# Performance work log

Measured on AMD Instinct MI355X. Metric: run time of the kernel, lower is better.

The kernel has to match this reference:

```python
import jax, jax.numpy as jnp
import numpy as np

N, E = 8000, 96000
S, V, G = 128, 64, 64          # scalar channels, l=1 vector channels, gate channels
LAT, OH = 128, 64
D = S + 3 * V                  # 320 feature dim per node/edge
AVG_NEIGH = 12.0
EPS = 1e-8

def _split(x):
    return x[:, :S], x[:, S:].reshape(x.shape[0], V, 3)

def sep_layernorm(x, ws, bs, wv):
    # separable LN: layernorm on l=0 scalars, component RMS norm on l=1 vectors
    s, v = _split(x)
    mu = jnp.mean(s, -1, keepdims=True)
    sc = s - mu
    s = sc * jax.lax.rsqrt(jnp.mean(sc * sc, -1, keepdims=True) + EPS) * ws + bs
    v = v * jax.lax.rsqrt(jnp.mean(v * v, (-2, -1), keepdims=True) + EPS) * wv[:, None]
    return s, v

def edge_frame(ev):
    # orthonormal frame with first axis along the edge (SO2 m=0 axis)
    a = ev * jax.lax.rsqrt(jnp.sum(ev * ev, -1, keepdims=True) + EPS)
    ref = jnp.where(jnp.abs(a[:, :1]) < 0.9,
                    jnp.array([1.0, 0.0, 0.0], ev.dtype),
                    jnp.array([0.0, 1.0, 0.0], ev.dtype))
    b = jnp.cross(a, ref)
    b = b * jax.lax.rsqrt(jnp.sum(b * b, -1, keepdims=True) + EPS)
    c = jnp.cross(a, b)
    return jnp.stack([a, b, c], axis=1)  # [E,3,3], rows are frame axes

def gate_act(s_all, v, n_s, n_g):
    s, g = s_all[:, :n_s], s_all[:, n_s:n_s + n_g]
    return jax.nn.silu(s), jax.nn.sigmoid(g)[:, :, None] * v

def e3_linear(s, v, ws, bs, wv):
    s = s @ ws * (1.0 / np.sqrt(s.shape[-1])) + bs
    v = jnp.einsum('eum,uk->ekm', v, wv) * (1.0 / np.sqrt(v.shape[1]))
    return s, v

def setup_inputs() -> dict:
    key = jax.random.key(0)
    ks = jax.random.split(key, 20)
    f = jnp.float32
    p = lambda k, sh: jax.random.normal(k, sh, f)
    inp = {}
    inp['latents'] = p(ks[0], (E, LAT))
    inp['node_features'] = p(ks[1], (N, D))
    inp['edge_features'] = p(ks[2], (E, D))
    at = jax.random.randint(ks[3], (N,), 0, OH)
    inp['atom_type'] = at
    inp['node_onehot'] = jax.nn.one_hot(at, OH, dtype=f)
    inp['edge_index'] = jax.random.randint(ks[4], (2, E), 0, N)
    inp['edge_vector'] = p(ks[5], (E, 3))
    inp['active_edges'] = jnp.arange(E)
    inp['sln_n_ws'] = jnp.ones((S,), f); inp['sln_n_bs'] = jnp.zeros((S,), f); inp['sln_n_wv'] = jnp.ones((V,), f)
    inp['sln_e_ws'] = jnp.ones((S,), f); inp['sln_e_bs'] = jnp.zeros((S,), f); inp['sln_e_wv'] = jnp.ones((V,), f)
    inp['so2_w0'] = p(ks[6], (3 * S + 3 * V, S + G + V))
    inp['so2_w1r'] = p(ks[7], (3 * V, V))
    inp['so2_w1i'] = p(ks[8], (3 * V, V))
    inp['env_w'] = p(ks[9], (LAT, S + V))
    inp['lp_ws'] = p(ks[10], (S, S)); inp['lp_bs'] = jnp.zeros((S,), f); inp['lp_wv'] = p(ks[11], (V, V))
    inp['oh_w_ss'] = p(ks[12], (S, OH, S))
    inp['oh_w_sg'] = p(ks[13], (S, OH, G))
    inp['oh_w_vv'] = p(ks[14], (V, OH, V))
    inp['ohl_ws'] = p(ks[15], (S, S)); inp['ohl_bs'] = jnp.zeros((S,), f); inp['ohl_wv'] = p(ks[16], (V, V))
    inp['res_param'] = jnp.zeros((1,), f)
    return inp

def reference(latents, node_features, edge_features, atom_type, node_onehot,
              edge_index, edge_vector, active_edges,
              sln_n_ws, sln_n_bs, sln_n_wv, sln_e_ws, sln_e_bs, sln_e_wv,
              so2_w0, so2_w1r, so2_w1i, env_w,
              lp_ws, lp_bs, lp_wv,
              oh_w_ss, oh_w_sg, oh_w_vv, ohl_ws, ohl_bs, ohl_wv, res_param):
    ctr = edge_index[0][active_edges]
    nbr = edge_index[1][active_edges]
    ns, nv = sep_layernorm(node_features, sln_n_ws, sln_n_bs, sln_n_wv)
    es, evf = sep_layernorm(edge_features, sln_e_ws, sln_e_bs, sln_e_wv)
    # concat center | edge | neighbor (scalars and vectors kept separate)
    sc = jnp.concatenate([ns[ctr], es, ns[nbr]], -1)          # [E, 3S]
    vc = jnp.concatenate([nv[ctr], evf, nv[nbr]], 1)          # [E, 3V, 3]
    R = edge_frame(edge_vector[active_edges])
    vf = jnp.einsum('eij,euj->eui', R, vc)                    # rotate into edge frame
    # SO2 linear: m=0 mixes scalars + on-axis components; m=+-1 mix with (re,im) weights
    m0_in = jnp.concatenate([sc, vf[:, :, 0]], -1)            # [E, 3S+3V]
    m0_out = m0_in @ so2_w0 * (1.0 / np.sqrt(m0_in.shape[-1]))  # [E, S+G+V]
    n1 = 1.0 / np.sqrt(vf.shape[1])
    vp = (vf[:, :, 1] @ so2_w1r - vf[:, :, 2] @ so2_w1i) * n1
    vm = (vf[:, :, 1] @ so2_w1i + vf[:, :, 2] @ so2_w1r) * n1
    v_out = jnp.stack([m0_out[:, S + G:], vp, vm], -1)        # [E,V,3] in frame
    v_out = jnp.einsum('eij,eui->euj', R, v_out)              # rotate back
    # gate activation + post linear
    ms, mv = gate_act(m0_out[:, :S + G], v_out, S, G)
    ms, mv = e3_linear(ms, mv, lp_ws, lp_bs, lp_wv)
    # env weighting (E3ElementLinear with weights from latents) + scatter to centers
    w = latents[active_edges] @ env_w * (1.0 / np.sqrt(LAT))  # [E, S+V]
    ms = ms * w[:, :S]
    mv = mv * w[:, S:, None]
    inv = 1.0 / np.sqrt(AVG_NEIGH)
    agg_s = jax.ops.segment_sum(ms, ctr, num_segments=N) * inv
    agg_v = jax.ops.segment_sum(mv, ctr, num_segments=N) * inv
    # one-hot FullyConnectedTensorProduct -> gate -> linear
    n_ss = 1.0 / np.sqrt(S * OH)
    n_vv = 1.0 / np.sqrt(V * OH)
    t_s = jnp.einsum('nu,nv,uvk->nk', agg_s, node_onehot, oh_w_ss) * n_ss
    t_g = jnp.einsum('nu,nv,uvk->nk', agg_s, node_onehot, oh_w_sg) * n_ss
    t_v = jnp.einsum('num,nv,uvk->nkm', agg_v, node_onehot, oh_w_vv) * n_vv
    gs, gv = gate_act(jnp.concatenate([t_s, t_g], -1), t_v, S, G)
    os_, ov = e3_linear(gs, gv, ohl_ws, ohl_bs, ohl_wv)
    new = jnp.concatenate([os_, ov.reshape(-1, 3 * V)], -1)
    # residual mixing (identity residual since node_irreps_in == irreps_out)
    alpha = jax.nn.sigmoid(res_param)[0]
    return alpha * node_features + (1.0 - alpha) * new
```

## Files before the change

### kernel.cpp

```cpp
#include <hip/hip_runtime.h>

#define EPS_LN 1e-8f

typedef __bf16 bf16x8 __attribute__((ext_vector_type(8)));
typedef float  f32x4  __attribute__((ext_vector_type(4)));

__device__ __forceinline__ float sigmoidf_(float x){ return 1.0f/(1.0f+__expf(-x)); }
__device__ __forceinline__ float siluf_(float x){ return x*sigmoidf_(x); }
__device__ __forceinline__ unsigned short f2bf(float x){ union{ __bf16 b; unsigned short u;} c; c.b = (__bf16)x; return c.u; }
__device__ __forceinline__ float bf2f(unsigned short u){ return __uint_as_float(((unsigned)u)<<16); }

union F4 { float4 v; float f[4]; };

__device__ __forceinline__ void st_bf4(char* base, int row, int stride_bytes, int k,
                                       float x0, float x1, float x2, float x3){
    union { __bf16 h[4]; unsigned long long u; } p;
    p.h[0]=(__bf16)x0; p.h[1]=(__bf16)x1; p.h[2]=(__bf16)x2; p.h[3]=(__bf16)x3;
    *(unsigned long long*)(base + row*stride_bytes + ((2*k) ^ ((row&7)<<4))) = p.u;
}
__device__ __forceinline__ bf16x8 ld_frag(const char* base, int row, int stride_bytes, int kbyte){
    return *(const bf16x8*)(base + row*stride_bytes + (kbyte ^ ((row&7)<<4)));
}
__device__ __forceinline__ void st_g4(__bf16* p, float x0, float x1, float x2, float x3){
    union { __bf16 h[4]; unsigned long long u; } pk;
    pk.h[0]=(__bf16)x0; pk.h[1]=(__bf16)x1; pk.h[2]=(__bf16)x2; pk.h[3]=(__bf16)x3;
    *(unsigned long long*)p = pk.u;
}
__device__ __forceinline__ uint4 pack8(float4 a, float4 b){
    union { __bf16 h[8]; uint4 u; } p;
    p.h[0]=(__bf16)a.x; p.h[1]=(__bf16)a.y; p.h[2]=(__bf16)a.z; p.h[3]=(__bf16)a.w;
    p.h[4]=(__bf16)b.x; p.h[5]=(__bf16)b.y; p.h[6]=(__bf16)b.z; p.h[7]=(__bf16)b.w;
    return p.u;
}
__device__ __forceinline__ int fm_idx(int n, int k, int NKT){
    return ((n>>4)*NKT + (k>>5))*512 + ((k>>3)&3)*128 + (n&15)*8 + (k&7);
}

__global__ void prep_weights(const float* __restrict__ w0,
                             const float* __restrict__ w1r, const float* __restrict__ w1i,
                             const float* __restrict__ env_w, const float* __restrict__ lp_ws,
                             const float* __restrict__ lp_wv,
                             __bf16* __restrict__ Wt, __bf16* __restrict__ w1rt, __bf16* __restrict__ w1it,
                             __bf16* __restrict__ Wfm, __bf16* __restrict__ Bvfm,
                             __bf16* __restrict__ envfm, __bf16* __restrict__ lpsfm,
                             __bf16* __restrict__ lpvfm)
{
    int t = blockIdx.x*256 + threadIdx.x;
    if (t < 576*256){
        int n = t/576, k = t%576;
        float v = w0[(size_t)k*256 + n];
        Wt[t] = (__bf16)v;
        Wfm[fm_idx(n,k,18)] = (__bf16)v;
    }
    if (t < 64*192){
        int c = t/192, k = t%192;
        w1rt[t] = (__bf16)w1r[(size_t)k*64 + c];
        w1it[t] = (__bf16)w1i[(size_t)k*64 + c];
    }
    if (t < 128*384){
        int n = t/384, k = t%384;
        float v;
        if (n < 64) v = (k<192) ? w1r[(size_t)k*64+n] : -w1i[(size_t)(k-192)*64+n];
        else        v = (k<192) ? w1i[(size_t)k*64+(n-64)] : w1r[(size_t)(k-192)*64+(n-64)];
        Bvfm[fm_idx(n,k,12)] = (__bf16)v;
    }
    if (t < 192*128){ int n=t/128, k=t%128; envfm[fm_idx(n,k,4)] = (__bf16)env_w[(size_t)k*192+n]; }
    if (t < 128*128){ int n=t/128, k=t%128; lpsfm[fm_idx(n,k,4)] = (__bf16)lp_ws[(size_t)k*128+n]; }
    if (t < 64*64)  { int n=t/64,  k=t%64;  lpvfm[fm_idx(n,k,2)] = (__bf16)lp_wv[(size_t)k*64+n]; }
}

__global__ void prep_oh(const float* __restrict__ oh_ss, const float* __restrict__ oh_sg,
                        const float* __restrict__ oh_vv,
                        __bf16* __restrict__ ssT, __bf16* __restrict__ sgT, __bf16* __restrict__ vvT)
{
    int t = blockIdx.x*256 + threadIdx.x;
    if (t < 64*128*128){
        int at = t / 16384;
        int r  = t & 16383;
        int u = r >> 7, k = r & 127;
        ssT[t] = (__bf16)oh_ss[((size_t)u*64 + at)*128 + k];
    }
    if (t < 64*128*64){
        int at = t / 8192;
        int r  = t & 8191;
        int u = r >> 6, k = r & 63;
        sgT[t] = (__bf16)oh_sg[((size_t)u*64 + at)*64 + k];
    }
    if (t < 64*64*64){
        int at = t / 4096;
        int r  = t & 4095;
        int u = r >> 6, k = r & 63;
        vvT[t] = (__bf16)oh_vv[((size_t)u*64 + at)*64 + k];
    }
}

__global__ void csr_count(const int* __restrict__ ei, const int* __restrict__ act,
                          int* __restrict__ cnt, int EA)
{
    int e = blockIdx.x*256 + threadIdx.x;
    if (e < EA) atomicAdd(&cnt[ei[act[e]]], 1);
}
__global__ void csr_scan(const int* __restrict__ cnt, int* __restrict__ offs,
                         int* __restrict__ cursor, int N)
{
    __shared__ int part[256];
    int t = threadIdx.x;
    int chunk = (N + 255) / 256;
    int lo = t*chunk, hi = lo+chunk; if (hi > N) hi = N; if (lo > N) lo = N;
    int s = 0;
    for (int i=lo;i<hi;i++) s += cnt[i];
    part[t] = s;
    __syncthreads();
    for (int d=1; d<256; d<<=1){
        int v = (t>=d) ? part[t-d] : 0;
        __syncthreads();
        part[t] += v;
        __syncthreads();
    }
    int run = (t==0) ? 0 : part[t-1];
    for (int i=lo;i<hi;i++){
        offs[i] = run; cursor[i] = run;
        run += cnt[i];
    }
    if (t==255) offs[N] = part[255];
}
__global__ void csr_fill(const int* __restrict__ ei, const int* __restrict__ act,
                         int* __restrict__ cursor, int* __restrict__ elist, int EA)
{
    int e = blockIdx.x*256 + threadIdx.x;
    if (e < EA){
        int n = ei[act[e]];
        int p = atomicAdd(&cursor[n], 1);
        elist[p] = e;
    }
}

__global__ void node_ln_kernel(const float* __restrict__ nf,
                               const float* __restrict__ ws, const float* __restrict__ bs,
                               const float* __restrict__ wv,
                               float* __restrict__ ns, float* __restrict__ nv, int N)
{
    int t = threadIdx.x;
    int lane = t & 63;
    int n = blockIdx.x*4 + (t>>6);
    if (n >= N) return;
    const float* row = nf + (size_t)n*320;
    float s0 = row[lane], s1 = row[64+lane];
    float sum = s0+s1, sq = s0*s0+s1*s1;
    #pragma unroll
    for (int m=1;m<64;m<<=1){ sum += __shfl_xor(sum,m,64); sq += __shfl_xor(sq,m,64); }
    float mu = sum*(1.0f/128.0f);
    float rs = rsqrtf(sq*(1.0f/128.0f) - mu*mu + EPS_LN);
    ns[(size_t)n*128+lane]    = (s0-mu)*rs*ws[lane]    + bs[lane];
    ns[(size_t)n*128+64+lane] = (s1-mu)*rs*ws[64+lane] + bs[64+lane];
    float v0 = row[128+lane], v1 = row[192+lane], v2 = row[256+lane];
    float vs = v0*v0+v1*v1+v2*v2;
    #pragma unroll
    for (int m=1;m<64;m<<=1) vs += __shfl_xor(vs,m,64);
    float rv = rsqrtf(vs*(1.0f/192.0f) + EPS_LN);
    nv[(size_t)n*192+lane]     = v0*rv*wv[lane/3];
    nv[(size_t)n*192+64+lane]  = v1*rv*wv[(64+lane)/3];
    nv[(size_t)n*192+128+lane] = v2*rv*wv[(128+lane)/3];
}

__global__ void stage_kernel(
    const float* __restrict__ ef_all,
    const int*   __restrict__ edge_index,
    const float* __restrict__ edge_vector,
    const int*   __restrict__ active_edges,
    const float* __restrict__ e_ws, const float* __restrict__ e_bs, const float* __restrict__ e_wv,
    const float* __restrict__ ns, const float* __restrict__ nv,
    __bf16* __restrict__ m0in, __bf16* __restrict__ vfg,
    float* __restrict__ Rg,
    int EA, int EF)
{
    int tid = blockIdx.x*256 + threadIdx.x;
    int e = tid >> 4, l = tid & 15;
    if (e >= EA) return;
    int ae = active_edges[e];
    int ct = edge_index[ae];
    int nb = edge_index[EF + ae];
    float ex = edge_vector[(size_t)ae*3+0];
    float ey = edge_vector[(size_t)ae*3+1];
    float ez = edge_vector[(size_t)ae*3+2];
    float rn = rsqrtf(ex*ex+ey*ey+ez*ez + EPS_LN);
    float ax = ex*rn, ay = ey*rn, az = ez*rn;
    float rx, ry;
    if (fabsf(ax) < 0.9f) { rx = 1.0f; ry = 0.0f; } else { rx = 0.0f; ry = 1.0f; }
    float bx = -az*ry, by = az*rx, bz = ax*ry - ay*rx;
    float bn = rsqrtf(bx*bx+by*by+bz*bz + EPS_LN);
    bx*=bn; by*=bn; bz*=bn;
    float cx = ay*bz - az*by;
    float cy = az*bx - ax*bz;
    float cz = ax*by - ay*bx;
    if (l == 0){
        float* Rr = Rg + (size_t)e*12;
        *(float4*)(Rr)   = make_float4(ax,ay,az,bx);
        *(float4*)(Rr+4) = make_float4(by,bz,cx,cy);
        *(float4*)(Rr+8) = make_float4(cz,0.f,0.f,0.f);
    }
    __bf16* Arow = m0in + (size_t)e*576;
    __bf16* V1r  = vfg + (size_t)e*384;
    __bf16* V2r  = V1r + 192;
    {
        const float4* pc4 = (const float4*)(ns + (size_t)ct*128);
        const float4* pn4 = (const float4*)(ns + (size_t)nb*128);
        F4 a,b2,c,d;
        a.v = pc4[l]; b2.v = pc4[16+l]; c.v = pn4[l]; d.v = pn4[16+l];
        st_g4(Arow + l*4,       a.f[0],a.f[1],a.f[2],a.f[3]);
        st_g4(Arow + 64 + l*4,  b2.f[0],b2.f[1],b2.f[2],b2.f[3]);
        st_g4(Arow + 256 + l*4, c.f[0],c.f[1],c.f[2],c.f[3]);
        st_g4(Arow + 320 + l*4, d.f[0],d.f[1],d.f[2],d.f[3]);
    }
    const float* ef = ef_all + (size_t)e*320;
    {
        F4 sa, sb;
        sa.v = *(const float4*)(ef + l*4);
        sb.v = *(const float4*)(ef + 64 + l*4);
        float sum=0.f, sq=0.f;
        #pragma unroll
        for (int i=0;i<4;i++){ sum += sa.f[i]+sb.f[i]; sq += sa.f[i]*sa.f[i]+sb.f[i]*sb.f[i]; }
        #pragma unroll
        for (int m=1;m<16;m<<=1){ sum += __shfl_xor(sum,m,64); sq += __shfl_xor(sq,m,64); }
        float mu = sum*(1.0f/128.0f);
        float rs = rsqrtf(sq*(1.0f/128.0f)-mu*mu + EPS_LN);
        float o0[4], o1[4];
        #pragma unroll
        for (int i=0;i<4;i++){
            int c0 = l*4+i, c1 = 64+l*4+i;
            o0[i] = (sa.f[i]-mu)*rs*e_ws[c0]+e_bs[c0];
            o1[i] = (sb.f[i]-mu)*rs*e_ws[c1]+e_bs[c1];
        }
        st_g4(Arow + 128 + l*4, o0[0],o0[1],o0[2],o0[3]);
        st_g4(Arow + 192 + l*4, o1[0],o1[1],o1[2],o1[3]);
    }
    {
        F4 va, vb, vc;
        va.v = *(const float4*)(ef + 128 + l*12);
        vb.v = *(const float4*)(ef + 128 + l*12 + 4);
        vc.v = *(const float4*)(ef + 128 + l*12 + 8);
        float vv[12];
        #pragma unroll
        for (int i=0;i<4;i++){ vv[i]=va.f[i]; vv[4+i]=vb.f[i]; vv[8+i]=vc.f[i]; }
        float sq=0.f;
        #pragma unroll
        for (int i=0;i<12;i++) sq += vv[i]*vv[i];
        #pragma unroll
        for (int m=1;m<16;m<<=1) sq += __shfl_xor(sq,m,64);
        float rv = rsqrtf(sq*(1.0f/192.0f) + EPS_LN);
        float f0[4], f1[4], f2[4];
        #pragma unroll
        for (int j=0;j<4;j++){
            int u = 4*l + j;
            float sc = rv * e_wv[u];
            float x = vv[3*j]*sc, y = vv[3*j+1]*sc, z = vv[3*j+2]*sc;
            f0[j] = ax*x+ay*y+az*z;
            f1[j] = bx*x+by*y+bz*z;
            f2[j] = cx*x+cy*y+cz*z;
        }
        st_g4(Arow + 384 + 64 + 4*l, f0[0],f0[1],f0[2],f0[3]);
        st_g4(V1r + 64 + 4*l, f1[0],f1[1],f1[2],f1[3]);
        st_g4(V2r + 64 + 4*l, f2[0],f2[1],f2[2],f2[3]);
    }
    {
        const float* pv = nv + (size_t)ct*192 + l*12;
        F4 va, vb, vc;
        va.v = *(const float4*)(pv);
        vb.v = *(const float4*)(pv+4);
        vc.v = *(const float4*)(pv+8);
        float vv[12];
        #pragma unroll
        for (int i=0;i<4;i++){ vv[i]=va.f[i]; vv[4+i]=vb.f[i]; vv[8+i]=vc.f[i]; }
        float f0[4], f1[4], f2[4];
        #pragma unroll
        for (int j=0;j<4;j++){
            float x = vv[3*j], y = vv[3*j+1], z = vv[3*j+2];
            f0[j] = ax*x+ay*y+az*z;
            f1[j] = bx*x+by*y+bz*z;
            f2[j] = cx*x+cy*y+cz*z;
        }
        st_g4(Arow + 384 + 4*l, f0[0],f0[1],f0[2],f0[3]);
        st_g4(V1r + 4*l, f1[0],f1[1],f1[2],f1[3]);
        st_g4(V2r + 4*l, f2[0],f2[1],f2[2],f2[3]);
    }
    {
        const float* pv = nv + (size_t)nb*192 + l*12;
        F4 va, vb, vc;
        va.v = *(const float4*)(pv);
        vb.v = *(const float4*)(pv+4);
        vc.v = *(const float4*)(pv+8);
        float vv[12];
        #pragma unroll
        for (int i=0;i<4;i++){ vv[i]=va.f[i]; vv[4+i]=vb.f[i]; vv[8+i]=vc.f[i]; }
        float f0[4], f1[4], f2[4];
        #pragma unroll
        for (int j=0;j<4;j++){
            float x = vv[3*j], y = vv[3*j+1], z = vv[3*j+2];
            f0[j] = ax*x+ay*y+az*z;
            f1[j] = bx*x+by*y+bz*z;
            f2[j] = cx*x+cy*y+cz*z;
        }
        st_g4(Arow + 384 + 128 + 4*l, f0[0],f0[1],f0[2],f0[3]);
        st_g4(V1r + 128 + 4*l, f1[0],f1[1],f1[2],f1[3]);
        st_g4(V2r + 128 + 4*l, f2[0],f2[1],f2[2],f2[3]);
    }
}

enum { EPI_PLAIN=0, EPI_LPS=1, EPI_LPV=2 };

template<int N, int K, int RT, int EPI, bool AGATHER>
__global__ __launch_bounds__((N/64)*RT*64)
void gemm_k(const __bf16* __restrict__ Ag, const float* __restrict__ Agf,
            const int* __restrict__ aidx,
            const __bf16* __restrict__ Bfm,
            unsigned short* __restrict__ outp,
            const unsigned short* __restrict__ wenv,
            const float* __restrict__ bias,
            float scale, int M)
{
    constexpr int NT  = N/64;
    constexpr int BM  = RT*64;
    constexpr int T   = NT*RT*64;
    constexpr int NKT = K/32;
    constexpr int NK  = K/64;
    constexpr int CA  = (BM*8 + T - 1)/T;
    __shared__ __align__(16) char lA[2][BM*128];

    const int tid  = threadIdx.x;
    const int brow = blockIdx.x*BM;
    const int mpl  = blockIdx.y;
    const __bf16* A = AGATHER ? nullptr : (Ag + (size_t)mpl*M*K);

    uint4 ra[CA];
    auto loadA = [&](int ks){
        #pragma unroll
        for (int i=0;i<CA;i++){
            int c = tid + i*T;
            if (c < BM*8){
                int r = c>>3;
                int gr = brow + r; if (gr >= M) gr = M-1;
                if constexpr (AGATHER){
                    int ae = aidx[gr];
                    const float* base = Agf + (size_t)ae*K + ks*64 + (c&7)*8;
                    float4 f0 = *(const float4*)(base);
                    float4 f1 = *(const float4*)(base+4);
                    ra[i] = pack8(f0, f1);
                } else {
                    ra[i] = *(const uint4*)((const char*)(A + (size_t)gr*K + ks*64) + (c&7)*16);
                }
            }
        }
    };
    auto storeA = [&](int buf){
        #pragma unroll
        for (int i=0;i<CA;i++){
            int c = tid + i*T;
            if (c < BM*8){
                int r = c>>3, off = (c&7)*16;
                *(uint4*)(&lA[buf][r*128 + (off ^ ((r&7)<<4))]) = ra[i];
            }
        }
    };

    const int wid = tid>>6, ln = tid&63;
    const int cc = ln & 15, gq = ln >> 4;
    const int wn = wid % NT, wm = wid / NT;
    const __bf16* bbase = Bfm + ((size_t)wn*4*NKT)*512 + (size_t)ln*8;

    f32x4 acc[4][4];
    #pragma unroll
    for (int i=0;i<4;i++)
        #pragma unroll
        for (int j=0;j<4;j++) acc[i][j] = (f32x4){0,0,0,0};

    loadA(0); storeA(0);
    int cur = 0;
    for (int ks=0; ks<NK; ks++){
        __syncthreads();
        if (ks+1 < NK) loadA(ks+1);
        #pragma unroll
        for (int kt2=0;kt2<2;kt2++){
            const int kt = ks*2 + kt2;
            const int kb = kt2*64 + 16*gq;
            bf16x8 af[4];
            #pragma unroll
            for (int mf=0;mf<4;mf++){
                int r = wm*64 + mf*16 + cc;
                af[mf] = *(const bf16x8*)(&lA[cur][r*128 + (kb ^ ((r&7)<<4))]);
            }
            #pragma unroll
            for (int nf=0;nf<4;nf++){
                bf16x8 bfr = *(const bf16x8*)(bbase + ((size_t)nf*NKT + kt)*512);
                #pragma unroll
                for (int mf=0;mf<4;mf++)
                    acc[mf][nf] = __builtin_amdgcn_mfma_f32_16x16x32_bf16(af[mf], bfr, acc[mf][nf], 0,0,0);
            }
        }
        if (ks+1 < NK) storeA(cur^1);
        cur ^= 1;
    }

    const float inv_avg_ = 0.288675134595f;
    #pragma unroll
    for (int mf=0;mf<4;mf++){
        #pragma unroll
        for (int nf=0;nf<4;nf++){
            #pragma unroll
            for (int j=0;j<4;j++){
                int gr = brow + wm*64 + mf*16 + gq*4 + j;
                if (gr >= M) continue;
                int col = wn*64 + nf*16 + cc;
                float v = acc[mf][nf][j];
                if constexpr (EPI == EPI_PLAIN){
                    outp[(size_t)gr*N + col] = f2bf(v*scale);
                } else if constexpr (EPI == EPI_LPS){
                    float val = (v*scale + bias[col]) * bf2f(wenv[(size_t)gr*192 + col]) * inv_avg_;
                    outp[(size_t)gr*320 + col] = f2bf(val);
                } else {
                    float val = v*0.125f * bf2f(wenv[(size_t)gr*192 + 128 + col]) * inv_avg_;
                    outp[(size_t)gr*320 + 128 + mpl*64 + col] = f2bf(val);
                }
            }
        }
    }
}

__global__ void mid_kernel(const unsigned short* __restrict__ m0out,
                           const unsigned short* __restrict__ vpvm,
                           const float* __restrict__ Rg,
                           unsigned short* __restrict__ As,
                           unsigned short* __restrict__ MVp, int EA)
{
    int tid = blockIdx.x*256 + threadIdx.x;
    int e = tid>>6, u = tid&63;
    if (e >= EA) return;
    float rl = (u < 12) ? Rg[(size_t)e*12 + u] : 0.f;
    float R0=__shfl(rl,0,64), R1=__shfl(rl,1,64), R2=__shfl(rl,2,64);
    float R3=__shfl(rl,3,64), R4=__shfl(rl,4,64), R5=__shfl(rl,5,64);
    float R6=__shfl(rl,6,64), R7=__shfl(rl,7,64), R8=__shfl(rl,8,64);
    const unsigned short* mo = m0out + (size_t)e*256;
    float s0 = bf2f(mo[192 + u]);
    float gt = sigmoidf_(bf2f(mo[128 + u]));
    float p  = bf2f(vpvm[(size_t)e*128 + u]);
    float q  = bf2f(vpvm[(size_t)e*128 + 64 + u]);
    size_t eu = (size_t)e*64 + u;
    size_t P  = (size_t)EA*64;
    MVp[eu]       = f2bf(gt*(R0*s0 + R3*p + R6*q));
    MVp[P + eu]   = f2bf(gt*(R1*s0 + R4*p + R7*q));
    MVp[2*P + eu] = f2bf(gt*(R2*s0 + R5*p + R8*q));
    As[(size_t)e*128 + u]      = f2bf(siluf_(bf2f(mo[u])));
    As[(size_t)e*128 + 64 + u] = f2bf(siluf_(bf2f(mo[64 + u])));
}

__launch_bounds__(256, 3)
__global__ void edge_kernel_fused(
    const float* __restrict__ latents,
    const float* __restrict__ ef_all,
    const int*   __restrict__ edge_index,
    const float* __restrict__ edge_vector,
    const int*   __restrict__ active_edges,
    const float* __restrict__ e_ws, const float* __restrict__ e_bs, const float* __restrict__ e_wv,
    const __bf16* __restrict__ Wt,
    const __bf16* __restrict__ w1rt,
    const __bf16* __restrict__ w1it,
    const float* __restrict__ env_w,
    const float* __restrict__ lp_ws, const float* __restrict__ lp_bs, const float* __restrict__ lp_wv,
    const float* __restrict__ ns, const float* __restrict__ nv,
    unsigned short* __restrict__ eout,
    int EA, int EF)
{
    __shared__ __align__(16) char smem[46592];
    char* sAbC = smem;
    char* sVFC = smem + 18432;
    float* sO  = (float*)smem;
    float* MV  = (float*)(smem + 16640);
    float* WE  = (float*)(smem + 33280);
    float* sR  = (float*)(smem + 45824);

    const int t = threadIdx.x;
    const int g = t >> 4, l = t & 15;
    const int e = blockIdx.x*16 + g;
    const bool act = (e < EA);

    int ct = 0, ae = 0;

    if (act) {
        ae = active_edges[e];
        ct = edge_index[ae];
        int nb = edge_index[EF + ae];
        float ex = edge_vector[(size_t)ae*3+0];
        float ey = edge_vector[(size_t)ae*3+1];
        float ez = edge_vector[(size_t)ae*3+2];
        float rn = rsqrtf(ex*ex+ey*ey+ez*ez + EPS_LN);
        float ax = ex*rn, ay = ey*rn, az = ez*rn;
        float rx, ry;
        if (fabsf(ax) < 0.9f) { rx = 1.0f; ry = 0.0f; } else { rx = 0.0f; ry = 1.0f; }
        float bx = -az*ry, by = az*rx, bz = ax*ry - ay*rx;
// ... 224 lines not shown
                        wacc[i]   += la.f[kk]*e0v.f[i];
                        wacc[4+i] += la.f[kk]*e1v.f[i];
                        wacc[8+i] += la.f[kk]*e2v.f[i];
                    }
                }
            }
            const float inv128 = 0.0883883476483f;
            #pragma unroll
            for (int i=0;i<12;i++) WE[g*196 + cc2 + i] = wacc[i]*inv128;
        }
    }
    __syncthreads();

    if (act) {
        const float inv_avg = 0.288675134595f;
        unsigned short* orow = eout + (size_t)e*320;
        {
            int c0 = l*8;
            float a8[8];
            #pragma unroll
            for (int i=0;i<8;i++) a8[i]=0.f;
            for (int k=0;k<128;k+=4){
                F4 av;
                av.v = *(const float4*)&sO[g*260 + k];
                #pragma unroll
                for (int kk=0;kk<4;kk++){
                    const float* wr = lp_ws + (size_t)(k+kk)*128 + c0;
                    F4 w0, w1_;
                    w0.v  = *(const float4*)(wr);
                    w1_.v = *(const float4*)(wr+4);
                    #pragma unroll
                    for (int i=0;i<4;i++){ a8[i] += av.f[kk]*w0.f[i]; a8[4+i] += av.f[kk]*w1_.f[i]; }
                }
            }
            const float s128 = 0.0883883476483f;
            union { unsigned short h[8]; uint4 u; } ps;
            #pragma unroll
            for (int i=0;i<8;i++){
                int c = c0+i;
                ps.h[i] = f2bf((a8[i]*s128 + lp_bs[c]) * WE[g*196 + c] * inv_avg);
            }
            *(uint4*)(orow + c0) = ps.u;
        }
        {
            int k0 = l*4;
            float av[4][3];
            #pragma unroll
            for (int j=0;j<4;j++)
                #pragma unroll
                for (int m2=0;m2<3;m2++) av[j][m2]=0.f;
            for (int u=0;u<64;u++){
                F4 wv4, mv4;
                wv4.v = *(const float4*)(lp_wv + (size_t)u*64 + k0);
                mv4.v = *(const float4*)&MV[g*260 + u*4];
                #pragma unroll
                for (int j=0;j<4;j++){
                    av[j][0] += wv4.f[j]*mv4.f[0];
                    av[j][1] += wv4.f[j]*mv4.f[1];
                    av[j][2] += wv4.f[j]*mv4.f[2];
                }
            }
            #pragma unroll
            for (int j=0;j<4;j++){
                int k = k0+j;
                float wk = WE[g*196 + 128 + k] * 0.125f * inv_avg;
                orow[128 +       k] = f2bf(av[j][0]*wk);
                orow[128 + 64  + k] = f2bf(av[j][1]*wk);
                orow[128 + 128 + k] = f2bf(av[j][2]*wk);
            }
        }
    }
}

__global__ void node_out_kernel(
    const float* __restrict__ nf,
    const int* __restrict__ atom_type,
    const int* __restrict__ offs, const int* __restrict__ elist,
    const unsigned short* __restrict__ eout,
    const __bf16* __restrict__ ssT, const __bf16* __restrict__ sgT, const __bf16* __restrict__ vvT,
    const float* __restrict__ ohl_ws, const float* __restrict__ ohl_bs, const float* __restrict__ ohl_wv,
    const float* __restrict__ res_param,
    float* __restrict__ out, int N)
{
    __shared__ float AGS[128];
    __shared__ float AGV[192];
    __shared__ float TSs[128];
    __shared__ float SG[64];
    __shared__ float TV[192];
    const int n = blockIdx.x;
    const int t = threadIdx.x;
    const int at = atom_type[n];

    {
        int lo = offs[n], hi = offs[n+1];
        float a0 = 0.f, a1 = 0.f;
        for (int i=lo;i<hi;i++){
            const unsigned short* row = eout + (size_t)elist[i]*320;
            a0 += bf2f(row[t]);
            if (t < 64) a1 += bf2f(row[256+t]);
        }
        if (t < 128) AGS[t] = a0;
        else { int idx = t-128; AGV[(idx&63)*3 + (idx>>6)] = a0; }
        if (t < 64) AGV[t*3+2] = a1;
    }
    __syncthreads();
    const float n_ss = 0.0110485434560f;
    const float n_vv = 0.015625f;
    if (t < 128) {
        const __bf16* w = ssT + (size_t)at*16384 + t;
        float acc = 0.0f;
        #pragma unroll 4
        for (int u=0;u<128;u++) acc += AGS[u]*(float)w[(size_t)u*128];
        TSs[t] = siluf_(acc*n_ss);
    } else if (t < 192) {
        int k = t-128;
        const __bf16* w = sgT + (size_t)at*8192 + k;
        float acc = 0.0f;
        #pragma unroll 4
        for (int u=0;u<128;u++) acc += AGS[u]*(float)w[(size_t)u*64];
        SG[k] = sigmoidf_(acc*n_ss);
    } else {
        int k = t-192;
        const __bf16* w = vvT + (size_t)at*4096 + k;
        float a0=0,a1=0,a2=0;
        #pragma unroll 4
        for (int u=0;u<64;u++){
            float wv = (float)w[(size_t)u*64];
            a0 += AGV[u*3+0]*wv;
            a1 += AGV[u*3+1]*wv;
            a2 += AGV[u*3+2]*wv;
        }
        TV[k*3+0]=a0*n_vv; TV[k*3+1]=a1*n_vv; TV[k*3+2]=a2*n_vv;
    }
    __syncthreads();
    const float alpha = sigmoidf_(res_param[0]);
    const float beta  = 1.0f - alpha;
    if (t < 128) {
        float acc = 0.0f;
        for (int k=0;k<128;k++) acc += TSs[k]*ohl_ws[(size_t)k*128 + t];
        float val = acc*0.0883883476483f + ohl_bs[t];
        out[(size_t)n*320 + t] = alpha*nf[(size_t)n*320 + t] + beta*val;
    } else if (t >= 192) {
        int k = t-192;
        float a0=0,a1=0,a2=0;
        for (int u=0;u<64;u++){
            float w = ohl_wv[(size_t)u*64 + k]*SG[u];
            a0 += TV[u*3+0]*w; a1 += TV[u*3+1]*w; a2 += TV[u*3+2]*w;
        }
        size_t base = (size_t)n*320 + 128 + (size_t)k*3;
        out[base+0] = alpha*nf[base+0] + beta*(a0*0.125f);
        out[base+1] = alpha*nf[base+1] + beta*(a1*0.125f);
        out[base+2] = alpha*nf[base+2] + beta*(a2*0.125f);
    }
}

extern "C" void kernel_launch(void* const* d_in, const int* in_sizes, int n_in,
                              void* d_out, int out_size, void* d_ws, size_t ws_size,
                              hipStream_t stream)
{
    const float* latents       = (const float*)d_in[0];
    const float* node_features = (const float*)d_in[1];
    const float* edge_features = (const float*)d_in[2];
    const int*   atom_type     = (const int*)d_in[3];
    const int*   edge_index    = (const int*)d_in[5];
    const float* edge_vector   = (const float*)d_in[6];
    const int*   active_edges  = (const int*)d_in[7];
    const float* sln_n_ws = (const float*)d_in[8];
    const float* sln_n_bs = (const float*)d_in[9];
    const float* sln_n_wv = (const float*)d_in[10];
    const float* sln_e_ws = (const float*)d_in[11];
    const float* sln_e_bs = (const float*)d_in[12];
    const float* sln_e_wv = (const float*)d_in[13];
    const float* so2_w0   = (const float*)d_in[14];
    const float* so2_w1r  = (const float*)d_in[15];
    const float* so2_w1i  = (const float*)d_in[16];
    const float* env_w    = (const float*)d_in[17];
    const float* lp_ws    = (const float*)d_in[18];
    const float* lp_bs    = (const float*)d_in[19];
    const float* lp_wv    = (const float*)d_in[20];
    const float* oh_w_ss  = (const float*)d_in[21];
    const float* oh_w_sg  = (const float*)d_in[22];
    const float* oh_w_vv  = (const float*)d_in[23];
    const float* ohl_ws   = (const float*)d_in[24];
    const float* ohl_bs   = (const float*)d_in[25];
    const float* ohl_wv   = (const float*)d_in[26];
    const float* res_param= (const float*)d_in[27];
    float* out = (float*)d_out;

    const int N  = in_sizes[1] / 320;
    const int EF = in_sizes[5] / 2;
    const int EA = in_sizes[7];

    char* p = (char*)d_ws;
    auto alloc = [&](size_t bytes) -> char* {
        char* r = p; p += (bytes + 255) & ~(size_t)255; return r;
    };
    float* ns      = (float*)alloc((size_t)N*128*4);
    float* nv      = (float*)alloc((size_t)N*192*4);
    int*   cnt     = (int*)  alloc((size_t)N*4);
    int*   offs    = (int*)  alloc(((size_t)N+1)*4);
    int*   cursor  = (int*)  alloc((size_t)N*4);
    int*   elist   = (int*)  alloc((size_t)EA*4);
    __bf16* Wt     = (__bf16*)alloc((size_t)576*256*2);
    __bf16* w1rt   = (__bf16*)alloc((size_t)64*192*2);
    __bf16* w1it   = (__bf16*)alloc((size_t)64*192*2);
    __bf16* Wfm    = (__bf16*)alloc((size_t)576*256*2);
    __bf16* Bvfm   = (__bf16*)alloc((size_t)128*384*2);
    __bf16* envfm  = (__bf16*)alloc((size_t)192*128*2);
    __bf16* lpsfm  = (__bf16*)alloc((size_t)128*128*2);
    __bf16* lpvfm  = (__bf16*)alloc((size_t)64*64*2);
    __bf16* ssT    = (__bf16*)alloc((size_t)64*128*128*2);
    __bf16* sgT    = (__bf16*)alloc((size_t)64*128*64*2);
    __bf16* vvT    = (__bf16*)alloc((size_t)64*64*64*2);
    unsigned short* eout = (unsigned short*)alloc((size_t)EA*320*2);
    float*  Rg    = (float*) alloc((size_t)EA*12*4);
    __bf16* m0in  = (__bf16*)alloc((size_t)EA*576*2);
    __bf16* vfg   = (__bf16*)alloc((size_t)EA*384*2);
    size_t split_need = (size_t)(p - (char*)d_ws);
    const bool use_split = (split_need <= ws_size);

    unsigned short* vpvm  = eout;
    unsigned short* m0out = (unsigned short*)vfg;
    unsigned short* As    = (unsigned short*)m0in;
    unsigned short* MVp   = As + (size_t)EA*128;
    unsigned short* w_env = MVp + (size_t)EA*192;

    hipMemsetAsync(cnt, 0, (size_t)N*sizeof(int), stream);
    prep_weights<<<576, 256, 0, stream>>>(so2_w0, so2_w1r, so2_w1i, env_w, lp_ws, lp_wv,
                                          Wt, w1rt, w1it, Wfm, Bvfm, envfm, lpsfm, lpvfm);
    prep_oh<<<4096, 256, 0, stream>>>(oh_w_ss, oh_w_sg, oh_w_vv, ssT, sgT, vvT);
    node_ln_kernel<<<(N+3)/4, 256, 0, stream>>>(node_features, sln_n_ws, sln_n_bs, sln_n_wv, ns, nv, N);
    csr_count<<<(EA+255)/256, 256, 0, stream>>>(edge_index, active_edges, cnt, EA);
    csr_scan<<<1, 256, 0, stream>>>(cnt, offs, cursor, N);
    csr_fill<<<(EA+255)/256, 256, 0, stream>>>(edge_index, active_edges, cursor, elist, EA);

    const float rn0    = 0.0416666666667f;
    const float n1     = 0.0721687836487f;
    const float inv128 = 0.0883883476483f;

    if (use_split){
        const int NB64  = (EA + 63) / 64;
        const int NB128 = (EA + 127) / 128;
        stage_kernel<<<(EA+15)/16, 256, 0, stream>>>(edge_features, edge_index, edge_vector, active_edges,
            sln_e_ws, sln_e_bs, sln_e_wv, ns, nv, m0in, vfg, Rg, EA, EF);
        gemm_k<128,384,2,EPI_PLAIN,false><<<dim3(NB128,1), 256, 0, stream>>>(
            vfg, nullptr, nullptr, Bvfm, vpvm, nullptr, nullptr, n1, EA);
        gemm_k<256,576,1,EPI_PLAIN,false><<<dim3(NB64,1), 256, 0, stream>>>(
            m0in, nullptr, nullptr, Wfm, m0out, nullptr, nullptr, rn0, EA);
        mid_kernel<<<(EA*64+255)/256, 256, 0, stream>>>(m0out, vpvm, Rg, As, MVp, EA);
        gemm_k<192,128,1,EPI_PLAIN,true><<<dim3(NB64,1), 192, 0, stream>>>(
            nullptr, latents, active_edges, envfm, w_env, nullptr, nullptr, inv128, EA);
        gemm_k<128,128,2,EPI_LPS,false><<<dim3(NB128,1), 256, 0, stream>>>(
            (const __bf16*)As, nullptr, nullptr, lpsfm, eout, w_env, lp_bs, inv128, EA);
        gemm_k<64,64,2,EPI_LPV,false><<<dim3(NB128,3), 128, 0, stream>>>(
            (const __bf16*)MVp, nullptr, nullptr, lpvfm, eout, w_env, nullptr, 0.125f, EA);
    } else {
        edge_kernel_fused<<<(EA+15)/16, 256, 0, stream>>>(latents, edge_features, edge_index, edge_vector, active_edges,
            sln_e_ws, sln_e_bs, sln_e_wv, Wt, w1rt, w1it, env_w, lp_ws, lp_bs, lp_wv,
            ns, nv, eout, EA, EF);
    }
    node_out_kernel<<<N, 256, 0, stream>>>(node_features, atom_type, offs, elist, eout,
        ssT, sgT, vvT, ohl_ws, ohl_bs, ohl_wv, res_param, out, N);
}
```

Baseline: 524.0 us.

## Precompute node-side GEMM contributions per node and shrink the edge m0 GEMM

The center and neighbor scalar rows of the m0 input are now multiplied by their slice of the weight once per node (N x 512 output) instead of once per edge. The edge GEMM then only covers K=320 and adds the gathered per-node partial products in its epilogue through new ct/nb index pairs. This cuts edge-GEMM FLOPs and the m0 input bandwidth, at the cost of an extra node GEMM and two gathered bf16 loads per output element. It also merges the two weight-prep kernels, makes the node aggregation load edge indices into shared memory and read rows as 32-bit pairs, and raises unroll factors.

```diff
diff --git a/kernel.cpp b/kernel.cpp
--- a/kernel.cpp
+++ b/kernel.cpp
@@ -36,21 +36,33 @@
     return ((n>>4)*NKT + (k>>5))*512 + ((k>>3)&3)*128 + (n&15)*8 + (k&7);
 }
 
-__global__ void prep_weights(const float* __restrict__ w0,
-                             const float* __restrict__ w1r, const float* __restrict__ w1i,
-                             const float* __restrict__ env_w, const float* __restrict__ lp_ws,
-                             const float* __restrict__ lp_wv,
-                             __bf16* __restrict__ Wt, __bf16* __restrict__ w1rt, __bf16* __restrict__ w1it,
-                             __bf16* __restrict__ Wfm, __bf16* __restrict__ Bvfm,
-                             __bf16* __restrict__ envfm, __bf16* __restrict__ lpsfm,
-                             __bf16* __restrict__ lpvfm)
+__global__ void prep_all(const float* __restrict__ w0,
+                         const float* __restrict__ w1r, const float* __restrict__ w1i,
+                         const float* __restrict__ env_w, const float* __restrict__ lp_ws,
+                         const float* __restrict__ lp_wv,
+                         const float* __restrict__ oh_ss, const float* __restrict__ oh_sg,
+                         const float* __restrict__ oh_vv,
+                         __bf16* __restrict__ Wt, __bf16* __restrict__ w1rt, __bf16* __restrict__ w1it,
+                         __bf16* __restrict__ Wevfm, __bf16* __restrict__ Bnodefm,
+                         __bf16* __restrict__ Bvfm,
+                         __bf16* __restrict__ envfm, __bf16* __restrict__ lpsfm,
+                         __bf16* __restrict__ lpvfm,
+                         __bf16* __restrict__ ssT, __bf16* __restrict__ sgT, __bf16* __restrict__ vvT)
 {
     int t = blockIdx.x*256 + threadIdx.x;
     if (t < 576*256){
         int n = t/576, k = t%576;
-        float v = w0[(size_t)k*256 + n];
-        Wt[t] = (__bf16)v;
-        Wfm[fm_idx(n,k,18)] = (__bf16)v;
+        Wt[t] = (__bf16)w0[(size_t)k*256 + n];
+    }
+    if (t < 256*320){
+        int n = t/320, k = t%320;
+        int src = (k<128) ? (128+k) : (384+(k-128));
+        Wevfm[fm_idx(n,k,10)] = (__bf16)w0[(size_t)src*256 + n];
+    }
+    if (t < 512*128){
+        int n = t/128, k = t%128;
+        float v = (n<256) ? w0[(size_t)k*256 + n] : w0[(size_t)(256+k)*256 + (n-256)];
+        Bnodefm[fm_idx(n,k,4)] = (__bf16)v;
     }
     if (t < 64*192){
         int c = t/192, k = t%192;
@@ -67,29 +79,16 @@
     if (t < 192*128){ int n=t/128, k=t%128; envfm[fm_idx(n,k,4)] = (__bf16)env_w[(size_t)k*192+n]; }
     if (t < 128*128){ int n=t/128, k=t%128; lpsfm[fm_idx(n,k,4)] = (__bf16)lp_ws[(size_t)k*128+n]; }
     if (t < 64*64)  { int n=t/64,  k=t%64;  lpvfm[fm_idx(n,k,2)] = (__bf16)lp_wv[(size_t)k*64+n]; }
-}
-
-__global__ void prep_oh(const float* __restrict__ oh_ss, const float* __restrict__ oh_sg,
-                        const float* __restrict__ oh_vv,
-                        __bf16* __restrict__ ssT, __bf16* __restrict__ sgT, __bf16* __restrict__ vvT)
-{
-    int t = blockIdx.x*256 + threadIdx.x;
     if (t < 64*128*128){
-        int at = t / 16384;
-        int r  = t & 16383;
-        int u = r >> 7, k = r & 127;
+        int at = t / 16384; int r = t & 16383; int u = r >> 7, k = r & 127;
         ssT[t] = (__bf16)oh_ss[((size_t)u*64 + at)*128 + k];
     }
     if (t < 64*128*64){
-        int at = t / 8192;
-        int r  = t & 8191;
-        int u = r >> 6, k = r & 63;
+        int at = t / 8192; int r = t & 8191; int u = r >> 6, k = r & 63;
         sgT[t] = (__bf16)oh_sg[((size_t)u*64 + at)*64 + k];
     }
     if (t < 64*64*64){
-        int at = t / 4096;
-        int r  = t & 4095;
-        int u = r >> 6, k = r & 63;
+        int at = t / 4096; int r = t & 4095; int u = r >> 6, k = r & 63;
         vvT[t] = (__bf16)oh_vv[((size_t)u*64 + at)*64 + k];
     }
 }
@@ -138,7 +137,8 @@
 __global__ void node_ln_kernel(const float* __restrict__ nf,
                                const float* __restrict__ ws, const float* __restrict__ bs,
                                const float* __restrict__ wv,
-                               float* __restrict__ ns, float* __restrict__ nv, int N)
+                               float* __restrict__ ns, float* __restrict__ nv,
+                               __bf16* __restrict__ nsb, int N)
 {
     int t = threadIdx.x;
     int lane = t & 63;
@@ -151,8 +151,12 @@
     for (int m=1;m<64;m<<=1){ sum += __shfl_xor(sum,m,64); sq += __shfl_xor(sq,m,64); }
     float mu = sum*(1.0f/128.0f);
     float rs = rsqrtf(sq*(1.0f/128.0f) - mu*mu + EPS_LN);
-    ns[(size_t)n*128+lane]    = (s0-mu)*rs*ws[lane]    + bs[lane];
-    ns[(size_t)n*128+64+lane] = (s1-mu)*rs*ws[64+lane] + bs[64+lane];
+    float o0 = (s0-mu)*rs*ws[lane]    + bs[lane];
+    float o1 = (s1-mu)*rs*ws[64+lane] + bs[64+lane];
+    ns[(size_t)n*128+lane]    = o0;
+    ns[(size_t)n*128+64+lane] = o1;
+    nsb[(size_t)n*128+lane]    = (__bf16)o0;
+    nsb[(size_t)n*128+64+lane] = (__bf16)o1;
     float v0 = row[128+lane], v1 = row[192+lane], v2 = row[256+lane];
     float vs = v0*v0+v1*v1+v2*v2;
     #pragma unroll
@@ -169,9 +173,10 @@
     const float* __restrict__ edge_vector,
     const int*   __restrict__ active_edges,
     const float* __restrict__ e_ws, const float* __restrict__ e_bs, const float* __restrict__ e_wv,
-    const float* __restrict__ ns, const float* __restrict__ nv,
-    __bf16* __restrict__ m0in, __bf16* __restrict__ vfg,
-    float* __restrict__ Rg,
+    const float* __restrict__ nv,
+    __bf16* __restrict__ m0in,
+    __bf16* __restrict__ vfg,
+    float* __restrict__ Rg, int2* __restrict__ ctnb,
     int EA, int EF)
 {
     int tid = blockIdx.x*256 + threadIdx.x;
@@ -198,20 +203,11 @@
         *(float4*)(Rr)   = make_float4(ax,ay,az,bx);
         *(float4*)(Rr+4) = make_float4(by,bz,cx,cy);
         *(float4*)(Rr+8) = make_float4(cz,0.f,0.f,0.f);
-    }
-    __bf16* Arow = m0in + (size_t)e*576;
+        ctnb[e] = make_int2(ct, nb);
+    }
+    __bf16* Arow = m0in + (size_t)e*320;
     __bf16* V1r  = vfg + (size_t)e*384;
     __bf16* V2r  = V1r + 192;
-    {
-        const float4* pc4 = (const float4*)(ns + (size_t)ct*128);
-        const float4* pn4 = (const float4*)(ns + (size_t)nb*128);
-        F4 a,b2,c,d;
-        a.v = pc4[l]; b2.v = pc4[16+l]; c.v = pn4[l]; d.v = pn4[16+l];
-        st_g4(Arow + l*4,       a.f[0],a.f[1],a.f[2],a.f[3]);
-        st_g4(Arow + 64 + l*4,  b2.f[0],b2.f[1],b2.f[2],b2.f[3]);
-        st_g4(Arow + 256 + l*4, c.f[0],c.f[1],c.f[2],c.f[3]);
-        st_g4(Arow + 320 + l*4, d.f[0],d.f[1],d.f[2],d.f[3]);
-    }
     const float* ef = ef_all + (size_t)e*320;
     {
         F4 sa, sb;
@@ -231,8 +227,8 @@
             o0[i] = (sa.f[i]-mu)*rs*e_ws[c0]+e_bs[c0];
             o1[i] = (sb.f[i]-mu)*rs*e_ws[c1]+e_bs[c1];
         }
-        st_g4(Arow + 128 + l*4, o0[0],o0[1],o0[2],o0[3]);
-        st_g4(Arow + 192 + l*4, o1[0],o1[1],o1[2],o1[3]);
+        st_g4(Arow + l*4,      o0[0],o0[1],o0[2],o0[3]);
+        st_g4(Arow + 64 + l*4, o1[0],o1[1],o1[2],o1[3]);
     }
     {
         F4 va, vb, vc;
@@ -258,7 +254,7 @@
             f1[j] = bx*x+by*y+bz*z;
             f2[j] = cx*x+cy*y+cz*z;
         }
-        st_g4(Arow + 384 + 64 + 4*l, f0[0],f0[1],f0[2],f0[3]);
+        st_g4(Arow + 128 + 64 + 4*l, f0[0],f0[1],f0[2],f0[3]);
         st_g4(V1r + 64 + 4*l, f1[0],f1[1],f1[2],f1[3]);
         st_g4(V2r + 64 + 4*l, f2[0],f2[1],f2[2],f2[3]);
     }
@@ -279,7 +275,7 @@
             f1[j] = bx*x+by*y+bz*z;
             f2[j] = cx*x+cy*y+cz*z;
         }
-        st_g4(Arow + 384 + 4*l, f0[0],f0[1],f0[2],f0[3]);
+        st_g4(Arow + 128 + 4*l, f0[0],f0[1],f0[2],f0[3]);
         st_g4(V1r + 4*l, f1[0],f1[1],f1[2],f1[3]);
         st_g4(V2r + 4*l, f2[0],f2[1],f2[2],f2[3]);
     }
@@ -300,13 +296,13 @@
             f1[j] = bx*x+by*y+bz*z;
             f2[j] = cx*x+cy*y+cz*z;
         }
-        st_g4(Arow + 384 + 128 + 4*l, f0[0],f0[1],f0[2],f0[3]);
+        st_g4(Arow + 128 + 128 + 4*l, f0[0],f0[1],f0[2],f0[3]);
         st_g4(V1r + 128 + 4*l, f1[0],f1[1],f1[2],f1[3]);
         st_g4(V2r + 128 + 4*l, f2[0],f2[1],f2[2],f2[3]);
     }
 }
 
-enum { EPI_PLAIN=0, EPI_LPS=1, EPI_LPV=2 };
+enum { EPI_PLAIN=0, EPI_LPS=1, EPI_LPV=2, EPI_MAINADD=3 };
 
 template<int N, int K, int RT, int EPI, bool AGATHER>
 __global__ __launch_bounds__((N/64)*RT*64)
@@ -316,6 +312,7 @@
             unsigned short* __restrict__ outp,
             const unsigned short* __restrict__ wenv,
             const float* __restrict__ bias,
+            const int2* __restrict__ ctnb, const __bf16* __restrict__ nodeCN,
             float scale, int M)
 {
     constexpr int NT  = N/64;
@@ -413,6 +410,11 @@
                 float v = acc[mf][nf][j];
                 if constexpr (EPI == EPI_PLAIN){
                     outp[(size_t)gr*N + col] = f2bf(v*scale);
+                } else if constexpr (EPI == EPI_MAINADD){
+                    int2 cn = ctnb[gr];
+                    float add = (float)nodeCN[(size_t)cn.x*512 + col]
+                              + (float)nodeCN[(size_t)cn.y*512 + 256 + col];
+                    outp[(size_t)gr*N + col] = f2bf((v + add)*scale);
                 } else if constexpr (EPI == EPI_LPS){
                     float val = (v*scale + bias[col]) * bf2f(wenv[(size_t)gr*192 + col]) * inv_avg_;
                     outp[(size_t)gr*320 + col] = f2bf(val);
@@ -803,6 +805,7 @@
     const float* __restrict__ res_param,
     float* __restrict__ out, int N)
 {
+    __shared__ int   sE[64];
     __shared__ float AGS[128];
     __shared__ float AGV[192];
     __shared__ float TSs[128];
@@ -811,18 +814,37 @@
     const int n = blockIdx.x;
     const int t = threadIdx.x;
     const int at = atom_type[n];
-
-    {
-        int lo = offs[n], hi = offs[n+1];
-        float a0 = 0.f, a1 = 0.f;
-        for (int i=lo;i<hi;i++){
-            const unsigned short* row = eout + (size_t)elist[i]*320;
-            a0 += bf2f(row[t]);
-            if (t < 64) a1 += bf2f(row[256+t]);
-        }
-        if (t < 128) AGS[t] = a0;
-        else { int idx = t-128; AGV[(idx&63)*3 + (idx>>6)] = a0; }
-        if (t < 64) AGV[t*3+2] = a1;
+    const int lo = offs[n], hi = offs[n+1];
+
+    float aLo = 0.f, aHi = 0.f;
+    for (int base = lo; base < hi; base += 64){
+        int cnt = hi - base; if (cnt > 64) cnt = 64;
+        __syncthreads();
+        if (t < cnt) sE[t] = elist[base + t];
+        __syncthreads();
+        if (t < 160){
+            int i = 0;
+            for (; i+4 <= cnt; i += 4){
+                unsigned x0 = *(const unsigned*)(eout + (size_t)sE[i  ]*320 + 2*t);
+                unsigned x1 = *(const unsigned*)(eout + (size_t)sE[i+1]*320 + 2*t);
+                unsigned x2 = *(const unsigned*)(eout + (size_t)sE[i+2]*320 + 2*t);
+                unsigned x3 = *(const unsigned*)(eout + (size_t)sE[i+3]*320 + 2*t);
+                aLo += bf2f((unsigned short)x0) + bf2f((unsigned short)x1)
+                     + bf2f((unsigned short)x2) + bf2f((unsigned short)x3);
+                aHi += bf2f((unsigned short)(x0>>16)) + bf2f((unsigned short)(x1>>16))
+                     + bf2f((unsigned short)(x2>>16)) + bf2f((unsigned short)(x3>>16));
+            }
+            for (; i < cnt; i++){
+                unsigned x = *(const unsigned*)(eout + (size_t)sE[i]*320 + 2*t);
+                aLo += bf2f((unsigned short)x);
+                aHi += bf2f((unsigned short)(x>>16));
+            }
+        }
+    }
+    if (t < 160){
+        int c0 = 2*t, c1 = 2*t+1;
+        if (c0 < 128) AGS[c0] = aLo; else { int d=c0-128; AGV[(d&63)*3 + (d>>6)] = aLo; }
+        if (c1 < 128) AGS[c1] = aHi; else { int d=c1-128; AGV[(d&63)*3 + (d>>6)] = aHi; }
     }
     __syncthreads();
     const float n_ss = 0.0110485434560f;
@@ -830,21 +852,21 @@
     if (t < 128) {
         const __bf16* w = ssT + (size_t)at*16384 + t;
         float acc = 0.0f;
-        #pragma unroll 4
+        #pragma unroll 8
         for (int u=0;u<128;u++) acc += AGS[u]*(float)w[(size_t)u*128];
         TSs[t] = siluf_(acc*n_ss);
     } else if (t < 192) {
         int k = t-128;
         const __bf16* w = sgT + (size_t)at*8192 + k;
         float acc = 0.0f;
-        #pragma unroll 4
+        #pragma unroll 8
         for (int u=0;u<128;u++) acc += AGS[u]*(float)w[(size_t)u*64];
         SG[k] = sigmoidf_(acc*n_ss);
     } else {
         int k = t-192;
         const __bf16* w = vvT + (size_t)at*4096 + k;
         float a0=0,a1=0,a2=0;
-        #pragma unroll 4
+        #pragma unroll 8
         for (int u=0;u<64;u++){
             float wv = (float)w[(size_t)u*64];
             a0 += AGV[u*3+0]*wv;
@@ -858,12 +880,14 @@
     const float beta  = 1.0f - alpha;
     if (t < 128) {
         float acc = 0.0f;
+        #pragma unroll 8
         for (int k=0;k<128;k++) acc += TSs[k]*ohl_ws[(size_t)k*128 + t];
         float val = acc*0.0883883476483f + ohl_bs[t];
         out[(size_t)n*320 + t] = alpha*nf[(size_t)n*320 + t] + beta*val;
     } else if (t >= 192) {
         int k = t-192;
         float a0=0,a1=0,a2=0;
+        #pragma unroll 8
         for (int u=0;u<64;u++){
             float w = ohl_wv[(size_t)u*64 + k]*SG[u];
             a0 += TV[u*3+0]*w; a1 += TV[u*3+1]*w; a2 += TV[u*3+2]*w;
@@ -918,6 +942,7 @@
     };
     float* ns      = (float*)alloc((size_t)N*128*4);
     float* nv      = (float*)alloc((size_t)N*192*4);
+    __bf16* nsb    = (__bf16*)alloc((size_t)N*128*2);
     int*   cnt     = (int*)  alloc((size_t)N*4);
     int*   offs    = (int*)  alloc(((size_t)N+1)*4);
     int*   cursor  = (int*)  alloc((size_t)N*4);
@@ -925,7 +950,8 @@
     __bf16* Wt     = (__bf16*)alloc((size_t)576*256*2);
     __bf16* w1rt   = (__bf16*)alloc((size_t)64*192*2);
     __bf16* w1it   = (__bf16*)alloc((size_t)64*192*2);
-    __bf16* Wfm    = (__bf16*)alloc((size_t)576*256*2);
+    __bf16* Wevfm  = (__bf16*)alloc((size_t)256*320*2);
+    __bf16* Bnodefm= (__bf16*)alloc((size_t)512*128*2);
     __bf16* Bvfm   = (__bf16*)alloc((size_t)128*384*2);
     __bf16* envfm  = (__bf16*)alloc((size_t)192*128*2);
     __bf16* lpsfm  = (__bf16*)alloc((size_t)128*128*2);
@@ -933,9 +959,12 @@
     __bf16* ssT    = (__bf16*)alloc((size_t)64*128*128*2);
     __bf16* sgT    = (__bf16*)alloc((size_t)64*128*64*2);
     __bf16* vvT    = (__bf16*)alloc((size_t)64*64*64*2);
+    __bf16* nodeCN = (__bf16*)alloc((size_t)N*512*2);
+    int2*  ctnb    = (int2*) alloc((size_t)EA*8);
     unsigned short* eout = (unsigned short*)alloc((size_t)EA*320*2);
+    unsigned short* w_env= (unsigned short*)alloc((size_t)EA*192*2);
     float*  Rg    = (float*) alloc((size_t)EA*12*4);
-    __bf16* m0in  = (__bf16*)alloc((size_t)EA*576*2);
+    __bf16* m0in  = (__bf16*)alloc((size_t)EA*320*2);
     __bf16* vfg   = (__bf16*)alloc((size_t)EA*384*2);
     size_t split_need = (size_t)(p - (char*)d_ws);
     const bool use_split = (split_need <= ws_size);
@@ -944,13 +973,13 @@
     unsigned short* m0out = (unsigned short*)vfg;
     unsigned short* As    = (unsigned short*)m0in;
     unsigned short* MVp   = As + (size_t)EA*128;
-    unsigned short* w_env = MVp + (size_t)EA*192;
 
     hipMemsetAsync(cnt, 0, (size_t)N*sizeof(int), stream);
-    prep_weights<<<576, 256, 0, stream>>>(so2_w0, so2_w1r, so2_w1i, env_w, lp_ws, lp_wv,
-                                          Wt, w1rt, w1it, Wfm, Bvfm, envfm, lpsfm, lpvfm);
-    prep_oh<<<4096, 256, 0, stream>>>(oh_w_ss, oh_w_sg, oh_w_vv, ssT, sgT, vvT);
-    node_ln_kernel<<<(N+3)/4, 256, 0, stream>>>(node_features, sln_n_ws, sln_n_bs, sln_n_wv, ns, nv, N);
+    prep_all<<<4096, 256, 0, stream>>>(so2_w0, so2_w1r, so2_w1i, env_w, lp_ws, lp_wv,
+                                       oh_w_ss, oh_w_sg, oh_w_vv,
+                                       Wt, w1rt, w1it, Wevfm, Bnodefm, Bvfm,
+                                       envfm, lpsfm, lpvfm, ssT, sgT, vvT);
+    node_ln_kernel<<<(N+3)/4, 256, 0, stream>>>(node_features, sln_n_ws, sln_n_bs, sln_n_wv, ns, nv, nsb, N);
     csr_count<<<(EA+255)/256, 256, 0, stream>>>(edge_index, active_edges, cnt, EA);
     csr_scan<<<1, 256, 0, stream>>>(cnt, offs, cursor, N);
     csr_fill<<<(EA+255)/256, 256, 0, stream>>>(edge_index, active_edges, cursor, elist, EA);
@@ -962,19 +991,22 @@
     if (use_split){
         const int NB64  = (EA + 63) / 64;
         const int NB128 = (EA + 127) / 128;
+        const int NBn   = (N + 63) / 64;
+        gemm_k<512,128,1,EPI_PLAIN,false><<<dim3(NBn,1), 512, 0, stream>>>(
+            nsb, nullptr, nullptr, Bnodefm, (unsigned short*)nodeCN, nullptr, nullptr, nullptr, nullptr, 1.0f, N);
         stage_kernel<<<(EA+15)/16, 256, 0, stream>>>(edge_features, edge_index, edge_vector, active_edges,
-            sln_e_ws, sln_e_bs, sln_e_wv, ns, nv, m0in, vfg, Rg, EA, EF);
+            sln_e_ws, sln_e_bs, sln_e_wv, nv, m0in, vfg, Rg, ctnb, EA, EF);
         gemm_k<128,384,2,EPI_PLAIN,false><<<dim3(NB128,1), 256, 0, stream>>>(
-            vfg, nullptr, nullptr, Bvfm, vpvm, nullptr, nullptr, n1, EA);
-        gemm_k<256,576,1,EPI_PLAIN,false><<<dim3(NB64,1), 256, 0, stream>>>(
-            m0in, nullptr, nullptr, Wfm, m0out, nullptr, nullptr, rn0, EA);
+            vfg, nullptr, nullptr, Bvfm, vpvm, nullptr, nullptr, nullptr, nullptr, n1, EA);
+        gemm_k<256,320,1,EPI_MAINADD,false><<<dim3(NB64,1), 256, 0, stream>>>(
+            m0in, nullptr, nullptr, Wevfm, m0out, nullptr, nullptr, ctnb, nodeCN, rn0, EA);
         mid_kernel<<<(EA*64+255)/256, 256, 0, stream>>>(m0out, vpvm, Rg, As, MVp, EA);
         gemm_k<192,128,1,EPI_PLAIN,true><<<dim3(NB64,1), 192, 0, stream>>>(
-            nullptr, latents, active_edges, envfm, w_env, nullptr, nullptr, inv128, EA);
+            nullptr, latents, active_edges, envfm, w_env, nullptr, nullptr, nullptr, nullptr, inv128, EA);
         gemm_k<128,128,2,EPI_LPS,false><<<dim3(NB128,1), 256, 0, stream>>>(
-            (const __bf16*)As, nullptr, nullptr, lpsfm, eout, w_env, lp_bs, inv128, EA);
+            (const __bf16*)As, nullptr, nullptr, lpsfm, eout, w_env, lp_bs, nullptr, nullptr, inv128, EA);
         gemm_k<64,64,2,EPI_LPV,false><<<dim3(NB128,3), 128, 0, stream>>>(
-            (const __bf16*)MVp, nullptr, nullptr, lpvfm, eout, w_env, nullptr, 0.125f, EA);
+            (const __bf16*)MVp, nullptr, nullptr, lpvfm, eout, w_env, nullptr, nullptr, nullptr, 0.125f, EA);
     } else {
         edge_kernel_fused<<<(EA+15)/16, 256, 0, stream>>>(latents, edge_features, edge_index, edge_vector, active_edges,
             sln_e_ws, sln_e_bs, sln_e_wv, Wt, w1rt, w1it, env_w, lp_ws, lp_bs, lp_wv,
```

Result: faster. 513.5 us (-2.0%).
